# Kernel optimization log

Hardware: AMD Instinct MI355X
Metric: run time of the kernel (lower is better)

Reference implementation:

```python
import jax, jax.numpy as jnp
import numpy as np
import math

B, S, D = 1, 4096, 2048
H, KVH, HD = 16, 4, 128
ROPE_THETA = 10000.0


def _rope_tables(seq_len, head_dim, theta):
    inv_freq = 1.0 / (theta ** (jnp.arange(0, head_dim, 2, dtype=jnp.float32) / head_dim))
    t = jnp.arange(seq_len, dtype=jnp.float32)
    freqs = jnp.outer(t, inv_freq)                      # [S, HD/2]
    emb = jnp.concatenate([freqs, freqs], axis=-1)      # [S, HD]
    return jnp.cos(emb)[None, None], jnp.sin(emb)[None, None]  # [1,1,S,HD]


def setup_inputs() -> dict:
    key = jax.random.key(0)
    ks = jax.random.split(key, 8)
    hidden_states = jax.random.normal(ks[0], (B, S, D), dtype=jnp.float32)
    # additive causal mask [B,1,S,S]
    neg = jnp.finfo(jnp.float32).min
    causal = jnp.where(jnp.tril(jnp.ones((S, S), dtype=bool)), 0.0, neg)
    attention_mask = jnp.broadcast_to(causal[None, None], (B, 1, S, S)).astype(jnp.float32)
    cos, sin = _rope_tables(S, HD, ROPE_THETA)
    gate = jax.random.uniform(ks[1], (B, S), dtype=jnp.float32, minval=0.05, maxval=1.0)
    sc = lambda fan_in: 1.0 / math.sqrt(fan_in)
    Wq = jax.random.normal(ks[2], (D, H * HD), dtype=jnp.float32) * sc(D)
    Wk = jax.random.normal(ks[3], (D, KVH * HD), dtype=jnp.float32) * sc(D)
    Wv = jax.random.normal(ks[4], (D, KVH * HD), dtype=jnp.float32) * sc(D)
    Wo = jax.random.normal(ks[5], (H * HD, D), dtype=jnp.float32) * sc(H * HD)
    return {"hidden_states": hidden_states, "attention_mask": attention_mask,
            "cos": cos, "sin": sin, "gate": gate,
            "Wq": Wq, "Wk": Wk, "Wv": Wv, "Wo": Wo}


def _rotate_half(x):
    h = x.shape[-1] // 2
    return jnp.concatenate([-x[..., h:], x[..., :h]], axis=-1)


def reference(hidden_states, attention_mask, cos, sin, gate, Wq, Wk, Wv, Wo):
    bsz, q_len, _ = hidden_states.shape
    # projections -> [B, heads, S, HD]
    q = (hidden_states @ Wq).reshape(bsz, q_len, H, HD).transpose(0, 2, 1, 3)
    k = (hidden_states @ Wk).reshape(bsz, q_len, KVH, HD).transpose(0, 2, 1, 3)
    v = (hidden_states @ Wv).reshape(bsz, q_len, KVH, HD).transpose(0, 2, 1, 3)
    # inline RoPE
    q = q * cos + _rotate_half(q) * sin
    k = k * cos + _rotate_half(k) * sin
    # GQA: repeat-interleave kv heads to match q heads
    g = H // KVH
    k = jnp.repeat(k, g, axis=1)
    v = jnp.repeat(v, g, axis=1)
    scores = jnp.einsum('bhqd,bhkd->bhqk', q, k) / math.sqrt(HD)
    scores = scores + attention_mask
    scores = scores + jnp.log(gate + 1e-8)[:, None, None, :]  # gate over kv positions
    weights = jax.nn.softmax(scores.astype(jnp.float32), axis=-1).astype(q.dtype)
    out = jnp.einsum('bhqk,bhkd->bhqd', weights, v)
    out = out.transpose(0, 2, 1, 3).reshape(bsz, q_len, H * HD)
    return out @ Wo
```

## Files before the change

### kernel.cpp

```cpp
#include <hip/hip_runtime.h>
#include <math.h>

#define S_LEN 4096
#define DMODEL 2048
#define NH 16
#define NKVH 4
#define HD 128
#define LDQKV 3072

typedef __attribute__((ext_vector_type(4))) float f32x4;
typedef __attribute__((ext_vector_type(8))) short bf16x8;
typedef __attribute__((ext_vector_type(4))) unsigned short us4;

static __device__ __forceinline__ unsigned short f2bf(float f) {
  unsigned int u = __builtin_bit_cast(unsigned int, f);
  u += 0x7fffu + ((u >> 16) & 1u);
  return (unsigned short)(u >> 16);
}
static __device__ __forceinline__ float bf2f(unsigned short h) {
  unsigned int u = ((unsigned int)h) << 16;
  return __builtin_bit_cast(float, u);
}
static __device__ __forceinline__ unsigned int cvt_pk_bf16(float lo, float hi) {
  unsigned int r;
  asm("v_cvt_pk_bf16_f32 %0, %1, %2" : "=v"(r) : "v"(lo), "v"(hi));
  return r;
}

#define GLDS16(g, l) __builtin_amdgcn_global_load_lds( \
    (__attribute__((address_space(1))) void*)(g), \
    (__attribute__((address_space(3))) void*)(l), 16, 0, 0)


__global__ __launch_bounds__(256) void k_cast_bf16(const float* __restrict__ src,
                                                   unsigned short* __restrict__ dst, int n4) {
  int i = blockIdx.x * 256 + threadIdx.x;
  if (i >= n4) return;
  const float4* s = (const float4*)src;
  float4 v = s[i];
  us4 o = { f2bf(v.x), f2bf(v.y), f2bf(v.z), f2bf(v.w) };
  *(us4*)(dst + (size_t)i * 4) = o;
}

__global__ __launch_bounds__(256) void k_transpose_bf16(const float* __restrict__ src,
    unsigned short* __restrict__ dst, int K, int N) {
  __shared__ float tile[64][65];
  int k0 = blockIdx.x * 64, n0 = blockIdx.y * 64;
  int t = threadIdx.x;
#pragma unroll
  for (int i = 0; i < 16; ++i) {
    int idx = t + i * 256;
    int r = idx >> 6, c = idx & 63;
    tile[r][c] = src[(size_t)(k0 + r) * N + n0 + c];
  }
  __syncthreads();
#pragma unroll
  for (int i = 0; i < 16; ++i) {
    int idx = t + i * 256;
    int r = idx >> 6, c = idx & 63;
    dst[(size_t)(n0 + r) * K + k0 + c] = f2bf(tile[c][r]);
  }
}

__global__ __launch_bounds__(256) void k_rope(unsigned short* __restrict__ QKV,
    const float* __restrict__ cp, const float* __restrict__ sp) {
  int gid = blockIdx.x * 256 + threadIdx.x;
  int d4 = (gid & 15) * 4;
  int hh = (gid >> 4) % 20;
  int s = gid / 320;
  int col = hh < NH ? hh * HD : DMODEL + (hh - NH) * HD;
  float qs = hh < NH ? 0.12751589341664477f : 1.0f;
  size_t base = (size_t)s * LDQKV + col + d4;
  us4 x1 = *(us4*)(QKV + base);
  us4 x2 = *(us4*)(QKV + base + 64);
  float4 c = *(const float4*)(cp + s * HD + d4);
  float4 sn = *(const float4*)(sp + s * HD + d4);
  us4 o1, o2;
  o1[0] = f2bf((bf2f(x1[0]) * c.x - bf2f(x2[0]) * sn.x) * qs);
  o1[1] = f2bf((bf2f(x1[1]) * c.y - bf2f(x2[1]) * sn.y) * qs);
  o1[2] = f2bf((bf2f(x1[2]) * c.z - bf2f(x2[2]) * sn.z) * qs);
  o1[3] = f2bf((bf2f(x1[3]) * c.w - bf2f(x2[3]) * sn.w) * qs);
  o2[0] = f2bf((bf2f(x2[0]) * c.x + bf2f(x1[0]) * sn.x) * qs);
  o2[1] = f2bf((bf2f(x2[1]) * c.y + bf2f(x1[1]) * sn.y) * qs);
  o2[2] = f2bf((bf2f(x2[2]) * c.z + bf2f(x1[2]) * sn.z) * qs);
  o2[3] = f2bf((bf2f(x2[3]) * c.w + bf2f(x1[3]) * sn.w) * qs);
  *(us4*)(QKV + base) = o1;
  *(us4*)(QKV + base + 64) = o2;
}

__global__ __launch_bounds__(256) void k_transpose_v(const unsigned short* __restrict__ QKV,
    unsigned short* __restrict__ Vt) {
  __shared__ unsigned short tile[64][72];
  int s0 = blockIdx.x * 64, c0 = blockIdx.y * 64;
  int t = threadIdx.x;
#pragma unroll
  for (int i = 0; i < 16; ++i) {
    int idx = t + i * 256;
    int r = idx >> 6, c = idx & 63;
    tile[r][c] = QKV[(size_t)(s0 + r) * LDQKV + DMODEL + NKVH * HD + c0 + c];
  }
  __syncthreads();
#pragma unroll
  for (int i = 0; i < 16; ++i) {
    int idx = t + i * 256;
    int r = idx >> 6, c = idx & 63;
    int pc = (c & 3) * 16 + (c >> 2);
    Vt[(size_t)(c0 + r) * S_LEN + s0 + c] = tile[pc][r];
  }
}


template<int OUTF32>
__global__ __launch_bounds__(256) void k_gemm_bt(
    const unsigned short* __restrict__ A, const unsigned short* __restrict__ Bt,
    void* __restrict__ Cp, int M, int N, int K) {
  __shared__ __attribute__((aligned(16))) unsigned short As[128 * 32];
  __shared__ __attribute__((aligned(16))) unsigned short Bs[128 * 32];
  const int t = threadIdx.x;
  const int wave = t >> 6, lane = t & 63;
  const int lr = lane & 15, lg = lane >> 4;
  const int bm = blockIdx.x * 128, bn = blockIdx.y * 128;
  const int wr = (wave >> 1) * 64, wc = (wave & 1) * 64;
  f32x4 acc[4][4];
#pragma unroll
  for (int i = 0; i < 4; ++i)
#pragma unroll
    for (int j = 0; j < 4; ++j) acc[i][j] = (f32x4){0.f, 0.f, 0.f, 0.f};

  for (int k0 = 0; k0 < K; k0 += 32) {
    __syncthreads();
#pragma unroll
    for (int i = 0; i < 2; ++i) {
      const int cb = (wave * 2 + i) * 64;
      const int c = cb + lane;
      const int row = c >> 2, kc = c & 3;
      const int ksw = (kc ^ (row & 3)) * 8;
      GLDS16(A + (size_t)(bm + row) * K + k0 + ksw, (char*)As + cb * 16);
      GLDS16(Bt + (size_t)(bn + row) * K + k0 + ksw, (char*)Bs + cb * 16);
    }
    asm volatile("s_waitcnt vmcnt(0)" ::: "memory");
    __syncthreads();
    bf16x8 af[4], bfr[4];
#pragma unroll
    for (int mi = 0; mi < 4; ++mi) {
      const int row = wr + mi * 16 + lr;
      af[mi] = *(const bf16x8*)(As + row * 32 + ((lg ^ (lr & 3)) * 8));
    }
#pragma unroll
    for (int ni = 0; ni < 4; ++ni) {
      const int row = wc + ni * 16 + lr;
      bfr[ni] = *(const bf16x8*)(Bs + row * 32 + ((lg ^ (lr & 3)) * 8));
    }
#pragma unroll
    for (int mi = 0; mi < 4; ++mi)
#pragma unroll
      for (int ni = 0; ni < 4; ++ni)
        acc[mi][ni] = __builtin_amdgcn_mfma_f32_16x16x32_bf16(af[mi], bfr[ni], acc[mi][ni], 0, 0, 0);
  }
#pragma unroll
  for (int mi = 0; mi < 4; ++mi)
#pragma unroll
    for (int ni = 0; ni < 4; ++ni)
#pragma unroll
      for (int r = 0; r < 4; ++r) {
        const int m = bm + wr + mi * 16 + lg * 4 + r;
        const int n = bn + wc + ni * 16 + lr;
        if (OUTF32) ((float*)Cp)[(size_t)m * N + n] = acc[mi][ni][r];
        else ((unsigned short*)Cp)[(size_t)m * N + n] = f2bf(acc[mi][ni][r]);
      }
}


#define STAGE_KV(kt_, buf_) do { \
  const int kv0_ = (kt_) * 128; \
  _Pragma("unroll") \
  for (int i_ = 0; i_ < 4; ++i_) { \
    const int cb_ = (wave * 4 + i_) * 64; \
    const int c_ = cb_ + lane; \
    const int row_ = c_ >> 4, kc_ = c_ & 15; \
    const int sw_ = (kc_ ^ (row_ & 7)) * 8; \
    GLDS16(Kp + (size_t)(kv0_ + row_) * LDQKV + sw_, (char*)Ks[buf_] + cb_ * 16); \
    GLDS16(Vp + (size_t)row_ * S_LEN + kv0_ + sw_, (char*)Vs[buf_] + cb_ * 16); \
  } \
} while (0)

__device__ __forceinline__ void qkt_one(const unsigned short* Kb,
    const bf16x8* qf, f32x4* sc, int lr, int lg) {
  __builtin_amdgcn_s_setprio(1);
#pragma unroll
  for (int cf = 0; cf < 8; ++cf) {
    sc[cf] = (f32x4){0.f, 0.f, 0.f, 0.f};
    const int row = cf * 16 + lr;
#pragma unroll
    for (int ks = 0; ks < 4; ++ks) {
      bf16x8 kb = *(const bf16x8*)(Kb + row * 128 + (((ks * 4 + lg) ^ (lr & 7)) * 8));
      sc[cf] = __builtin_amdgcn_mfma_f32_16x16x32_bf16(qf[ks], kb, sc[cf], 0, 0, 0);
    }
  }
  __builtin_amdgcn_s_setprio(0);
}

template<bool DIAG>
__device__ __forceinline__ void softmax_pv(
    f32x4* sc, const unsigned short* Vb, unsigned short (*PsW)[72],
    const float* g8, int kv0, int qbase,
    f32x4* acc, f32x4& acc_s, float* mrow, int lr, int lg,
    const bf16x8 vb_ones) {
  if (DIAG) {
#pragma unroll
    for (int cf = 0; cf < 8; ++cf) {
      const int kpos = kv0 + cf * 16 + lr;
#pragma unroll
      for (int r = 0; r < 4; ++r)
        sc[cf][r] = (kpos <= qbase + r) ? sc[cf][r] : -3e38f;
    }
  }
  float lmax[4];
#pragma unroll
  for (int r = 0; r < 4; ++r) {
    float a = fmaxf(fmaxf(sc[0][r], sc[1][r]), fmaxf(sc[2][r], sc[3][r]));
    float b = fmaxf(fmaxf(sc[4][r], sc[5][r]), fmaxf(sc[6][r], sc[7][r]));
    lmax[r] = fmaxf(a, b);
  }
  bool need = (lmax[0] > mrow[0] + 11.5416f) | (lmax[1] > mrow[1] + 11.5416f) |
              (lmax[2] > mrow[2] + 11.5416f) | (lmax[3] > mrow[3] + 11.5416f);
  if (__any(need)) {
    float tm[4] = {lmax[0], lmax[1], lmax[2], lmax[3]};
#pragma unroll
    for (int off = 8; off; off >>= 1)
#pragma unroll
      for (int r = 0; r < 4; ++r) tm[r] = fmaxf(tm[r], __shfl_xor(tm[r], off));
#pragma unroll
    for (int r = 0; r < 4; ++r) {
      const float mn = fmaxf(mrow[r], tm[r]);
      const float alpha = __builtin_amdgcn_exp2f(mrow[r] - mn);
      mrow[r] = mn;
#pragma unroll
      for (int j = 0; j < 8; ++j) acc[j][r] *= alpha;
      acc_s[r] *= alpha;
    }
  }
#pragma unroll
  for (int hh = 0; hh < 2; ++hh) {
    const f32x4* s4 = sc + hh * 4;
    const float* g4 = g8 + hh * 4;
#pragma unroll
    for (int r = 0; r < 4; ++r) {
      float p0 = __builtin_amdgcn_exp2f(s4[0][r] - mrow[r]) * g4[0];
      float p1 = __builtin_amdgcn_exp2f(s4[1][r] - mrow[r]) * g4[1];
      float p2 = __builtin_amdgcn_exp2f(s4[2][r] - mrow[r]) * g4[2];
      float p3 = __builtin_amdgcn_exp2f(s4[3][r] - mrow[r]) * g4[3];
      uint2 pk = { cvt_pk_bf16(p0, p1), cvt_pk_bf16(p2, p3) };
      *(uint2*)(&PsW[lg * 4 + r][lr * 4]) = pk;
    }
    asm volatile("s_waitcnt lgkmcnt(0)" ::: "memory");
    __builtin_amdgcn_sched_barrier(0);
    __builtin_amdgcn_s_setprio(1);
#pragma unroll
    for (int ks = 0; ks < 2; ++ks) {
      bf16x8 pa = *(const bf16x8*)(&PsW[lr][ks * 32 + lg * 8]);
#pragma unroll
      for (int j = 0; j < 8; ++j) {
        const int d = j * 16 + lr;
        bf16x8 vb = *(const bf16x8*)(Vb + d * 128 + ((hh * 8 + ((ks * 4 + lg) ^ (lr & 7))) * 8));
        acc[j] = __builtin_amdgcn_mfma_f32_16x16x32_bf16(pa, vb, acc[j], 0, 0, 0);
      }
      acc_s = __builtin_amdgcn_mfma_f32_16x16x32_bf16(pa, vb_ones, acc_s, 0, 0, 0);
    }
    __builtin_amdgcn_s_setprio(0);
  }
}

__global__ __launch_bounds__(512) void k_attn(
    const unsigned short* __restrict__ QKV, const unsigned short* __restrict__ Vt,
    const float* __restrict__ gate, unsigned short* __restrict__ Oattn) {
  __shared__ __attribute__((aligned(16))) unsigned short Ks[2][128 * 128];
  __shared__ __attribute__((aligned(16))) unsigned short Vs[2][128 * 128];
  __shared__ __attribute__((aligned(16))) unsigned short Ps[8][16][72];
  const int h = blockIdx.y, kvh = h >> 2;
  const int bx = blockIdx.x;
  const int t = threadIdx.x, wave = t >> 6, lane = t & 63;
  const int lr = lane & 15, lg = lane >> 4;
  const unsigned short* Qp = QKV + h * HD;
  const unsigned short* Kp = QKV + DMODEL + kvh * HD;
  const unsigned short* Vp = Vt + (size_t)kvh * HD * S_LEN;
  unsigned short (*PsW)[72] = Ps[wave];
  bf16x8 vb_ones;
  {
    const short one = (short)0x3F80, z = 0;
    const short e = (lr == 0) ? one : z;
    vb_ones = (bf16x8){e, e, e, e, e, e, e, e};
  }

  for (int half = 0; half < 2; ++half) {
    const int st = half ? bx : (31 - bx);
    const int q0 = st * 128;
    const int nt = st + 1;
    const int qbase = q0 + wave * 16 + lg * 4;

    bf16x8 qf[4];
    {
      const size_t qoff = (size_t)(q0 + wave * 16 + lr) * LDQKV;
#pragma unroll
      for (int ks = 0; ks < 4; ++ks)
        qf[ks] = *(const bf16x8*)(Qp + qoff + ks * 32 + lg * 8);
    }
    f32x4 acc[8];
#pragma unroll
    for (int j = 0; j < 8; ++j) acc[j] = (f32x4){0.f, 0.f, 0.f, 0.f};
    f32x4 acc_s = (f32x4){0.f, 0.f, 0.f, 0.f};
    float mrow[4] = {-3e38f, -3e38f, -3e38f, -3e38f};
    f32x4 sc[8];
    float g8[8];

    __builtin_amdgcn_s_barrier();
    STAGE_KV(0, 0);

    int kt = 0;
    for (; kt < nt - 1; ++kt) {
      STAGE_KV(kt + 1, (kt + 1) & 1);
      asm volatile("s_waitcnt vmcnt(8)" ::: "memory");
      __builtin_amdgcn_s_barrier();
#pragma unroll
      for (int cf = 0; cf < 8; ++cf) g8[cf] = gate[kt * 128 + cf * 16 + lr];
      qkt_one(Ks[kt & 1], qf, sc, lr, lg);
      softmax_pv<false>(sc, Vs[kt & 1], PsW, g8, kt * 128, qbase, acc, acc_s, mrow, lr, lg, vb_ones);
      __builtin_amdgcn_s_barrier();
    }
    {
      asm volatile("s_waitcnt vmcnt(0)" ::: "memory");
      __builtin_amdgcn_s_barrier();
#pragma unroll
      for (int cf = 0; cf < 8; ++cf) g8[cf] = gate[kt * 128 + cf * 16 + lr];
      qkt_one(Ks[kt & 1], qf, sc, lr, lg);
      softmax_pv<true>(sc, Vs[kt & 1], PsW, g8, kt * 128, qbase, acc, acc_s, mrow, lr, lg, vb_ones);
    }

    float inv[4];
#pragma unroll
    for (int r = 0; r < 4; ++r)
      inv[r] = 1.0f / __shfl(acc_s[r], lane & 48);
#pragma unroll
    for (int j = 0; j < 8; ++j)
#pragma unroll
      for (int r = 0; r < 4; ++r)
        Oattn[(size_t)(qbase + r) * DMODEL + h * HD + j * 16 + lr] = f2bf(acc[j][r] * inv[r]);
  }
}


extern "C" void kernel_launch(void* const* d_in, const int* in_sizes, int n_in,
                              void* d_out, int out_size, void* d_ws, size_t ws_size,
                              hipStream_t stream) {
  (void)in_sizes; (void)n_in; (void)out_size; (void)ws_size;
  const float* hid  = (const float*)d_in[0];
  const float* cosp = (const float*)d_in[2];
  const float* sinp = (const float*)d_in[3];
  const float* gate = (const float*)d_in[4];
  const float* Wq   = (const float*)d_in[5];
  const float* Wk   = (const float*)d_in[6];
  const float* Wv   = (const float*)d_in[7];
  const float* Wo   = (const float*)d_in[8];
  float* out = (float*)d_out;
  char* ws = (char*)d_ws;
  unsigned short* Xb   = (unsigned short*)(ws);
  unsigned short* Wt   = (unsigned short*)(ws + (size_t)16777216);
  unsigned short* Wot  = (unsigned short*)(ws + (size_t)29360128);
  unsigned short* QKV  = (unsigned short*)(ws + (size_t)37748736);
  unsigned short* Oatt = (unsigned short*)(ws + (size_t)62914560);
  unsigned short* Vt   = (unsigned short*)(ws + (size_t)79691776);

  k_cast_bf16<<<8192, 256, 0, stream>>>(hid, Xb, 2097152);
  k_transpose_bf16<<<dim3(32, 32), 256, 0, stream>>>(Wq, Wt, 2048, 2048);
  k_transpose_bf16<<<dim3(32, 8), 256, 0, stream>>>(Wk, Wt + (size_t)2048 * 2048, 2048, 512);
  k_transpose_bf16<<<dim3(32, 8), 256, 0, stream>>>(Wv, Wt + (size_t)2560 * 2048, 2048, 512);
  k_transpose_bf16<<<dim3(32, 32), 256, 0, stream>>>(Wo, Wot, 2048, 2048);
  k_gemm_bt<0><<<dim3(32, 24), 256, 0, stream>>>(Xb, Wt, QKV, 4096, 3072, 2048);
  k_rope<<<5120, 256, 0, stream>>>(QKV, cosp, sinp);
  k_transpose_v<<<dim3(64, 8), 256, 0, stream>>>(QKV, Vt);
  k_attn<<<dim3(16, 16), 512, 0, stream>>>(QKV, Vt, gate, Oatt);
  k_gemm_bt<1><<<dim3(32, 16), 256, 0, stream>>>(Oatt, Wot, out, 4096, 2048, 2048);
}
```

Measured before the change: 269.0 us.

## Replace GEMM with 256x128 triple-buffered pipelined kernel using 8 waves

After: 281.0 us. 1.04x slower.

```diff
diff --git a/kernel.cpp b/kernel.cpp
--- a/kernel.cpp
+++ b/kernel.cpp
@@ -110,53 +110,168 @@
 }
 
 
+#define MFMA16(a, b, c) __builtin_amdgcn_mfma_f32_16x16x32_bf16(a, b, c, 0, 0, 0)
+
+template<bool DO_STAGE, int VM>
+__device__ __forceinline__ void gemm_ktile(
+    const unsigned short* __restrict__ Ac, const unsigned short* __restrict__ Bc,
+    const unsigned short* __restrict__ Ag, const unsigned short* __restrict__ Bg,
+    char* Astg, char* Bstg, int K,
+    f32x4 (&acc)[4][4], int lr, int lg, int wr, int wc, int wave, int srow, int gsel) {
+  bf16x8 aq[2][2], b0q[2][2], b1q[2][2];
+  const int gbase = ((lg) ^ (lr & 7));
+  (void)gbase;
+#pragma unroll
+  for (int f = 0; f < 2; ++f) {
+    const int ra = wr + f * 16 + lr;
+    const int rb = wc + f * 16 + lr;
+#pragma unroll
+    for (int ks = 0; ks < 2; ++ks) {
+      aq[f][ks]  = *(const bf16x8*)(Ac + ra * 64 + (((ks * 4 + lg) ^ (lr & 7)) * 8));
+      b0q[f][ks] = *(const bf16x8*)(Bc + rb * 64 + (((ks * 4 + lg) ^ (lr & 7)) * 8));
+    }
+  }
+  if (DO_STAGE) {
+#pragma unroll
+    for (int j = 0; j < 2; ++j) {
+      const int row = j * 64 + srow;
+      GLDS16(Ag + (size_t)row * K + ((gsel ^ (row & 7)) * 8), Astg + (j * 8192 + wave * 1024));
+    }
+  }
+  __builtin_amdgcn_s_barrier();
+  __builtin_amdgcn_s_setprio(1);
+#pragma unroll
+  for (int mf = 0; mf < 2; ++mf)
+#pragma unroll
+    for (int nf = 0; nf < 2; ++nf)
+#pragma unroll
+      for (int ks = 0; ks < 2; ++ks)
+        acc[mf][nf] = MFMA16(aq[mf][ks], b0q[nf][ks], acc[mf][nf]);
+  __builtin_amdgcn_s_setprio(0);
+  __builtin_amdgcn_s_barrier();
+#pragma unroll
+  for (int f = 0; f < 2; ++f) {
+    const int rb = wc + 32 + f * 16 + lr;
+#pragma unroll
+    for (int ks = 0; ks < 2; ++ks)
+      b1q[f][ks] = *(const bf16x8*)(Bc + rb * 64 + (((ks * 4 + lg) ^ (lr & 7)) * 8));
+  }
+  if (DO_STAGE) {
+#pragma unroll
+    for (int j = 0; j < 2; ++j) {
+      const int row = 128 + j * 64 + srow;
+      GLDS16(Ag + (size_t)row * K + ((gsel ^ (row & 7)) * 8), Astg + (16384 + j * 8192 + wave * 1024));
+    }
+  }
+  __builtin_amdgcn_s_barrier();
+  __builtin_amdgcn_s_setprio(1);
+#pragma unroll
+  for (int mf = 0; mf < 2; ++mf)
+#pragma unroll
+    for (int nf = 0; nf < 2; ++nf)
+#pragma unroll
+      for (int ks = 0; ks < 2; ++ks)
+        acc[mf][2 + nf] = MFMA16(aq[mf][ks], b1q[nf][ks], acc[mf][2 + nf]);
+  __builtin_amdgcn_s_setprio(0);
+  __builtin_amdgcn_s_barrier();
+#pragma unroll
+  for (int f = 0; f < 2; ++f) {
+    const int ra = wr + 32 + f * 16 + lr;
+#pragma unroll
+    for (int ks = 0; ks < 2; ++ks)
+      aq[f][ks] = *(const bf16x8*)(Ac + ra * 64 + (((ks * 4 + lg) ^ (lr & 7)) * 8));
+  }
+  if (DO_STAGE) {
+#pragma unroll
+    for (int j = 0; j < 2; ++j) {
+      const int row = j * 64 + srow;
+      GLDS16(Bg + (size_t)row * K + ((gsel ^ (row & 7)) * 8), Bstg + (j * 8192 + wave * 1024));
+    }
+  }
+  __builtin_amdgcn_s_barrier();
+  __builtin_amdgcn_s_setprio(1);
+#pragma unroll
+  for (int mf = 0; mf < 2; ++mf)
+#pragma unroll
+    for (int nf = 0; nf < 2; ++nf)
+#pragma unroll
+      for (int ks = 0; ks < 2; ++ks)
+        acc[2 + mf][2 + nf] = MFMA16(aq[mf][ks], b1q[nf][ks], acc[2 + mf][2 + nf]);
+  __builtin_amdgcn_s_setprio(0);
+  __builtin_amdgcn_s_barrier();
+  __builtin_amdgcn_s_setprio(1);
+#pragma unroll
+  for (int mf = 0; mf < 2; ++mf)
+#pragma unroll
+    for (int nf = 0; nf < 2; ++nf)
+#pragma unroll
+      for (int ks = 0; ks < 2; ++ks)
+        acc[2 + mf][nf] = MFMA16(aq[mf][ks], b0q[nf][ks], acc[2 + mf][nf]);
+  __builtin_amdgcn_s_setprio(0);
+  if (VM == 6)      asm volatile("s_waitcnt vmcnt(6)" ::: "memory");
+  else if (VM == 0) asm volatile("s_waitcnt vmcnt(0)" ::: "memory");
+  __builtin_amdgcn_s_barrier();
+}
+
 template<int OUTF32>
-__global__ __launch_bounds__(256) void k_gemm_bt(
+__global__ __launch_bounds__(512, 1) void k_gemm8(
     const unsigned short* __restrict__ A, const unsigned short* __restrict__ Bt,
-    void* __restrict__ Cp, int M, int N, int K) {
-  __shared__ __attribute__((aligned(16))) unsigned short As[128 * 32];
-  __shared__ __attribute__((aligned(16))) unsigned short Bs[128 * 32];
-  const int t = threadIdx.x;
-  const int wave = t >> 6, lane = t & 63;
+    void* __restrict__ Cp, int M, int N, int K, int nbm, int nbn) {
+  __shared__ __attribute__((aligned(16))) unsigned short Ab[3][256 * 64];
+  __shared__ __attribute__((aligned(16))) unsigned short Bb[3][128 * 64];
+  const int t = threadIdx.x, wave = t >> 6, lane = t & 63;
   const int lr = lane & 15, lg = lane >> 4;
-  const int bm = blockIdx.x * 128, bn = blockIdx.y * 128;
+  const int srow = wave * 8 + (lane >> 3);
+  const int gsel = lane & 7;
+  const int nwg = nbm * nbn;
+  const int q8 = nwg >> 3;
+  const int wg = (blockIdx.x & 7) * q8 + (blockIdx.x >> 3);
+  const int bm = (wg % nbm) * 256, bn = (wg / nbm) * 128;
   const int wr = (wave >> 1) * 64, wc = (wave & 1) * 64;
+
   f32x4 acc[4][4];
 #pragma unroll
   for (int i = 0; i < 4; ++i)
 #pragma unroll
     for (int j = 0; j < 4; ++j) acc[i][j] = (f32x4){0.f, 0.f, 0.f, 0.f};
 
-  for (int k0 = 0; k0 < K; k0 += 32) {
-    __syncthreads();
-#pragma unroll
-    for (int i = 0; i < 2; ++i) {
-      const int cb = (wave * 2 + i) * 64;
-      const int c = cb + lane;
-      const int row = c >> 2, kc = c & 3;
-      const int ksw = (kc ^ (row & 3)) * 8;
-      GLDS16(A + (size_t)(bm + row) * K + k0 + ksw, (char*)As + cb * 16);
-      GLDS16(Bt + (size_t)(bn + row) * K + k0 + ksw, (char*)Bs + cb * 16);
-    }
-    asm volatile("s_waitcnt vmcnt(0)" ::: "memory");
-    __syncthreads();
-    bf16x8 af[4], bfr[4];
-#pragma unroll
-    for (int mi = 0; mi < 4; ++mi) {
-      const int row = wr + mi * 16 + lr;
-      af[mi] = *(const bf16x8*)(As + row * 32 + ((lg ^ (lr & 3)) * 8));
-    }
-#pragma unroll
-    for (int ni = 0; ni < 4; ++ni) {
-      const int row = wc + ni * 16 + lr;
-      bfr[ni] = *(const bf16x8*)(Bs + row * 32 + ((lg ^ (lr & 3)) * 8));
-    }
-#pragma unroll
-    for (int mi = 0; mi < 4; ++mi)
-#pragma unroll
-      for (int ni = 0; ni < 4; ++ni)
-        acc[mi][ni] = __builtin_amdgcn_mfma_f32_16x16x32_bf16(af[mi], bfr[ni], acc[mi][ni], 0, 0, 0);
-  }
+#pragma unroll
+  for (int tt = 0; tt < 2; ++tt) {
+#pragma unroll
+    for (int u = 0; u < 2; ++u)
+#pragma unroll
+      for (int j = 0; j < 2; ++j) {
+        const int row = u * 128 + j * 64 + srow;
+        GLDS16(A + (size_t)(bm + row) * K + tt * 64 + ((gsel ^ (row & 7)) * 8),
+               (char*)Ab[tt] + u * 16384 + j * 8192 + wave * 1024);
+      }
+#pragma unroll
+    for (int j = 0; j < 2; ++j) {
+      const int row = j * 64 + srow;
+      GLDS16(Bt + (size_t)(bn + row) * K + tt * 64 + ((gsel ^ (row & 7)) * 8),
+             (char*)Bb[tt] + j * 8192 + wave * 1024);
+    }
+  }
+  asm volatile("s_waitcnt vmcnt(6)" ::: "memory");
+  __builtin_amdgcn_s_barrier();
+
+  const unsigned short *a0 = Ab[0], *a1 = Ab[1], *a2 = Ab[2];
+  const unsigned short *b0 = Bb[0], *b1 = Bb[1], *b2 = Bb[2];
+  const int nkt = K >> 6;
+  for (int kt = 0; kt < nkt - 2; ++kt) {
+    gemm_ktile<true, 6>(a0, b0,
+        A + (size_t)bm * K + (kt + 2) * 64, Bt + (size_t)bn * K + (kt + 2) * 64,
+        (char*)a2, (char*)b2, K, acc, lr, lg, wr, wc, wave, srow, gsel);
+    const unsigned short* ta = a0; a0 = a1; a1 = a2; a2 = ta;
+    const unsigned short* tb = b0; b0 = b1; b1 = b2; b2 = tb;
+  }
+  gemm_ktile<false, 0>(a0, b0, A, Bt, (char*)a2, (char*)b2, K, acc, lr, lg, wr, wc, wave, srow, gsel);
+  {
+    const unsigned short* ta = a0; a0 = a1; a1 = a2; a2 = ta;
+    const unsigned short* tb = b0; b0 = b1; b1 = b2; b2 = tb;
+  }
+  gemm_ktile<false, -1>(a0, b0, A, Bt, (char*)a2, (char*)b2, K, acc, lr, lg, wr, wc, wave, srow, gsel);
+
 #pragma unroll
   for (int mi = 0; mi < 4; ++mi)
 #pragma unroll
@@ -375,9 +490,9 @@
   k_transpose_bf16<<<dim3(32, 8), 256, 0, stream>>>(Wk, Wt + (size_t)2048 * 2048, 2048, 512);
   k_transpose_bf16<<<dim3(32, 8), 256, 0, stream>>>(Wv, Wt + (size_t)2560 * 2048, 2048, 512);
   k_transpose_bf16<<<dim3(32, 32), 256, 0, stream>>>(Wo, Wot, 2048, 2048);
-  k_gemm_bt<0><<<dim3(32, 24), 256, 0, stream>>>(Xb, Wt, QKV, 4096, 3072, 2048);
+  k_gemm8<0><<<384, 512, 0, stream>>>(Xb, Wt, QKV, 4096, 3072, 2048, 16, 24);
   k_rope<<<5120, 256, 0, stream>>>(QKV, cosp, sinp);
   k_transpose_v<<<dim3(64, 8), 256, 0, stream>>>(QKV, Vt);
   k_attn<<<dim3(16, 16), 512, 0, stream>>>(QKV, Vt, gate, Oatt);
-  k_gemm_bt<1><<<dim3(32, 16), 256, 0, stream>>>(Oatt, Wot, out, 4096, 2048, 2048);
-}
+  k_gemm8<1><<<256, 512, 0, stream>>>(Oatt, Wot, out, 4096, 2048, 2048, 16, 16);
+}
```
